# Kernel optimization log

Measured on AMD Instinct MI355X. Metric: run time of the kernel, lower is better.

Reference implementation:

```python
import jax, jax.numpy as jnp
import numpy as np
from jax import lax

KS = [3, 5, 7, 9]
DS = [1, 2, 3, 4]
BN_EPS = 1e-5


def setup_inputs() -> dict:
    key = jax.random.key(0)
    ks = jax.random.split(key, 16)
    B, Cin, H, W = 16, 64, 256, 256
    Ce = 64  # out_channels // 2
    inp = {"x": jax.random.normal(ks[0], (B, Cin, H, W), jnp.float32)}
    for i, (k, _) in enumerate(zip(KS, DS)):
        fan_in = Cin * k * k
        inp[f"w{i}"] = jax.random.normal(ks[1 + i], (Ce, Cin, k, k), jnp.float32) / np.sqrt(fan_in)
        inp[f"b{i}"] = jnp.zeros((Ce,), jnp.float32)
    inp["bn_scale"] = jnp.ones((4, Ce), jnp.float32)
    inp["bn_bias"] = jnp.zeros((4, Ce), jnp.float32)
    inp["bn_mean"] = jax.random.normal(ks[5], (4, Ce), jnp.float32) * 0.1
    inp["bn_var"] = jax.random.uniform(ks[6], (4, Ce), jnp.float32, 0.5, 1.5)
    inp["gate_w"] = jax.random.normal(ks[7], (4, Cin), jnp.float32) / np.sqrt(Cin)
    inp["gate_b"] = jnp.zeros((4,), jnp.float32)
    return inp


def _expert(x, w, b, scale, bias, mean, var, k, d):
    pad = d * (k - 1) // 2
    y = lax.conv_general_dilated(
        x, w, window_strides=(2, 2), padding=[(pad, pad), (pad, pad)],
        rhs_dilation=(d, d), dimension_numbers=("NCHW", "OIHW", "NCHW"))
    y = y + b[None, :, None, None]
    inv = scale * lax.rsqrt(var + BN_EPS)
    y = y * inv[None, :, None, None] + (bias - mean * inv)[None, :, None, None]
    return jax.nn.gelu(y, approximate=False)


def reference(x, w0, b0, w1, b1, w2, b2, w3, b3,
              bn_scale, bn_bias, bn_mean, bn_var, gate_w, gate_b):
    B = x.shape[0]
    # Gate: global average pool -> linear -> softmax -> top-2 renormalized
    pooled = x.mean(axis=(2, 3))                    # (B, Cin)
    gates = jax.nn.softmax(pooled @ gate_w.T + gate_b, axis=1)  # (B, 4)
    top2_w, top2_idx = lax.top_k(gates, 2)
    top2_w = top2_w / (top2_w.sum(axis=1, keepdims=True) + 1e-8)
    # Dense compute of all 4 experts (faithful to original module)
    ws, bs = [w0, w1, w2, w3], [b0, b1, b2, b3]
    outs = [
        _expert(x, ws[i], bs[i], bn_scale[i], bn_bias[i], bn_mean[i], bn_var[i], KS[i], DS[i])
        for i in range(4)
    ]
    E = jnp.stack(outs, axis=1)                     # (B, 4, Ce, H/2, W/2)
    sel = jnp.take_along_axis(E, top2_idx[:, :, None, None, None], axis=1)  # (B,2,Ce,h,w)
    weighted = sel * top2_w[:, :, None, None, None]
    # concat top-2 along channel dim == reshape (B,2,Ce,h,w) -> (B,2*Ce,h,w)
    Bc, two, Ce, h, w = weighted.shape
    return weighted.reshape(Bc, two * Ce, h, w)
```

## Files before the change

### kernel.cpp

```cpp
#include <hip/hip_runtime.h>
#include <hip/hip_bf16.h>
#include <math.h>

#define CIN 64
#define CE  64
#define HH  256
#define WW  256
#define OHW 128
#define PW  288
#define PH  288
#define WOFF 19600
#define TOFF (WOFF + 6144)

typedef __attribute__((ext_vector_type(8))) short bf16x8;
typedef __attribute__((ext_vector_type(4))) float f32x4;

static __device__ __forceinline__ unsigned short f2bf(float f) {
    __hip_bfloat16 h = __float2bfloat16(f);
    return *reinterpret_cast<unsigned short*>(&h);
}

#define GLOAD16(gsrc, ldst)                                                        \
    __builtin_amdgcn_global_load_lds(                                              \
        (const __attribute__((address_space(1))) void*)(gsrc),                     \
        (__attribute__((address_space(3))) void*)(ldst), 16, 0, 0)

template <bool PRE>
__global__ __launch_bounds__(256)
void poolcvt_kernel(const float* __restrict__ x, unsigned short* __restrict__ xbf,
                    float* __restrict__ partial) {
    int blk = blockIdx.x;
    int rc = blockIdx.y;
    int tid = threadIdx.x, lane = tid & 63, wv = tid >> 6;
    int c0 = lane * 4;
    const float* xb = x + (size_t)blk * 8 * (HH * WW);
    unsigned short* pl = xbf + (size_t)blk * (PW * PH) * 8;
    float s[8];
#pragma unroll
    for (int j = 0; j < 8; ++j) s[j] = 0.f;
#pragma unroll 1
    for (int rr = wv; rr < 32; rr += 4) {
        int h = rc * 32 + rr;
        float4 v[8];
#pragma unroll
        for (int j = 0; j < 8; ++j)
            v[j] = *reinterpret_cast<const float4*>(xb + (size_t)j * (HH * WW) + h * WW + c0);
#pragma unroll
        for (int j = 0; j < 8; ++j) s[j] += (v[j].x + v[j].y) + (v[j].z + v[j].w);
        if (PRE) {
            size_t o16 = ((size_t)(16 + h) * PW + 16 + c0);
            unsigned short u[4][8];
#pragma unroll
            for (int j = 0; j < 8; ++j) {
                u[0][j] = f2bf(v[j].x);
                u[1][j] = f2bf(v[j].y);
                u[2][j] = f2bf(v[j].z);
                u[3][j] = f2bf(v[j].w);
            }
#pragma unroll
            for (int cc = 0; cc < 4; ++cc)
                *reinterpret_cast<bf16x8*>(pl + (o16 + cc) * 8) =
                    *reinterpret_cast<const bf16x8*>(u[cc]);
        }
    }
    if (PRE) {
        bf16x8 z = (bf16x8)(short)0;
#pragma unroll 1
        for (int i = tid; i < 32 * 32; i += 256) {
            int rr = i >> 5, cc = i & 31;
            int pr = 16 + rc * 32 + rr;
            int pc = (cc < 16) ? cc : (256 + cc);
            *reinterpret_cast<bf16x8*>(pl + ((size_t)pr * PW + pc) * 8) = z;
        }
        if (rc == 0) {
#pragma unroll 1
            for (int i = tid; i < 16 * PW; i += 256)
                *reinterpret_cast<bf16x8*>(pl + (size_t)i * 8) = z;
        }
        if (rc == 7) {
#pragma unroll 1
            for (int i = tid; i < 16 * PW; i += 256)
                *reinterpret_cast<bf16x8*>(pl + ((size_t)(272 * PW) + i) * 8) = z;
        }
    }
#pragma unroll
    for (int j = 0; j < 8; ++j) {
#pragma unroll
        for (int m = 32; m >= 1; m >>= 1) s[j] += __shfl_xor(s[j], m, 64);
    }
    __shared__ float red[4][8];
    if (lane == 0) {
#pragma unroll
        for (int j = 0; j < 8; ++j) red[wv][j] = s[j];
    }
    __syncthreads();
    if (tid < 8) {
        int j = tid;
        float t = (red[0][j] + red[1][j]) + (red[2][j] + red[3][j]);
        partial[(blk * 8 + rc) * 8 + j] = t;
    }
}

__global__ __launch_bounds__(64)
void gate_kernel(const float* __restrict__ partial, const float* __restrict__ gw,
                 const float* __restrict__ gb, int* __restrict__ sel_idx,
                 float* __restrict__ sel_w) {
    int b = blockIdx.x;
    int c = threadIdx.x;
    float p = 0.f;
#pragma unroll
    for (int rc = 0; rc < 8; ++rc)
        p += partial[(((b * 8 + (c >> 3)) * 8) + rc) * 8 + (c & 7)];
    p *= (1.0f / (HH * WW));
    float l[4];
#pragma unroll
    for (int e = 0; e < 4; ++e) l[e] = p * gw[e * CIN + c];
#pragma unroll
    for (int m = 32; m >= 1; m >>= 1) {
#pragma unroll
        for (int e = 0; e < 4; ++e) l[e] += __shfl_xor(l[e], m, 64);
    }
    if (c == 0) {
        float g[4], s = 0.f;
#pragma unroll
        for (int e = 0; e < 4; ++e) l[e] += gb[e];
        float mx = fmaxf(fmaxf(l[0], l[1]), fmaxf(l[2], l[3]));
#pragma unroll
        for (int e = 0; e < 4; ++e) { g[e] = expf(l[e] - mx); s += g[e]; }
#pragma unroll
        for (int e = 0; e < 4; ++e) g[e] /= s;
        int i1 = 0;
        for (int e = 1; e < 4; ++e) if (g[e] > g[i1]) i1 = e;
        int i2 = -1;
        for (int e = 0; e < 4; ++e) {
            if (e == i1) continue;
            if (i2 < 0 || g[e] > g[i2]) i2 = e;
        }
        float den = g[i1] + g[i2] + 1e-8f;
        sel_idx[b * 2 + 0] = i1;
        sel_idx[b * 2 + 1] = i2;
        sel_w[b * 2 + 0] = g[i1] / den;
        sel_w[b * 2 + 1] = g[i2] / den;
    }
}

__global__ void order_kernel(const int* __restrict__ sel_idx, int* __restrict__ ord) {
    if (threadIdx.x == 0) {
        int pos = 0;
        const int pri[4] = {3, 2, 1, 0};
        for (int pi = 0; pi < 4; ++pi)
            for (int bs = 0; bs < 32; ++bs)
                if (sel_idx[bs] == pri[pi]) ord[pos++] = bs;
    }
}

__global__ __launch_bounds__(256)
void wprep_all_kernel(const float* __restrict__ w0, const float* __restrict__ w1,
                      const float* __restrict__ w2, const float* __restrict__ w3,
                      unsigned short* __restrict__ wq) {
    int cb = blockIdx.x;
    int y = blockIdx.y;
    const float* w;
    int g0, k, GE;
    size_t base;
    if (y < 3)       { w = w0; g0 = y;      k = 3; GE = 3;  base = 0; }
    else if (y < 10) { w = w1; g0 = y - 3;  k = 5; GE = 7;  base = 49152; }
    else if (y < 23) { w = w2; g0 = y - 10; k = 7; GE = 13; base = 163840; }
    else             { w = w3; g0 = y - 23; k = 9; GE = 21; base = 376832; }
    int k2 = k * k;
    int t = threadIdx.x, tl = t >> 6, co = t & 63;
    int tap = g0 * 4 + tl;
    unsigned short vals[8];
#pragma unroll
    for (int j = 0; j < 8; ++j) {
        float v = 0.f;
        if (tap < k2) v = w[(size_t)(co * CIN + cb * 8 + j) * k2 + tap];
        vals[j] = f2bf(v);
    }
    *reinterpret_cast<bf16x8*>(&wq[base + (size_t)(cb * GE + g0) * 2048 + t * 8]) =
        *reinterpret_cast<const bf16x8*>(vals);
}

template <int K, int D, int GE, bool EVEN, bool PRE>
__device__ __forceinline__ void conv_body(const float* __restrict__ xb,
                                          const unsigned short* __restrict__ xpb,
                                          const unsigned short* __restrict__ wq,
                                          unsigned short* __restrict__ lds,
                                          f32x4 acc[4][4],
                                          int ih0, int iw0, int lane, int wv, int tid) {
    constexpr int K2 = K * K;
    constexpr int TS = 31 + (K - 1) * D;
    constexpr int S = (TS + 1) / 2;
    constexpr int HPW = S * 8;
    constexpr int PITCH = 2 * HPW;
    constexpr int NRC = (TS + 1) / 2;
    constexpr int NEL = EVEN ? NRC * NRC : TS * 2 * S;
    constexpr int ITER = (NEL + 255) / 256;
    constexpr int DH = EVEN ? D / 2 : 0;
    constexpr size_t PLANE = (size_t)PW * PH * 8;
    constexpr int RSTEP = EVEN ? NRC * 16 : PITCH * 4;
    int p = lane & 15, hi = lane >> 4;

    if constexpr (PRE) {
        int gofs[ITER];
#pragma unroll
        for (int i = 0; i < ITER; ++i) {
            int idx = tid + i * 256;
            if (idx > NEL - 1) idx = NEL - 1;
            int ih, iw;
            if constexpr (EVEN) {
                int r = idx / NRC, c = idx - r * NRC;
                ih = ih0 + 16 + 2 * r;
                iw = iw0 + 16 + 2 * c;
            } else {
                int r = idx / (2 * S), rem = idx - r * (2 * S);
                int half = rem >= S ? 1 : 0;
                int sl = rem - half * S;
                int c = 2 * sl + half;
                if (c > TS - 1) c = TS - 1;
                ih = ih0 + 16 + r;
                iw = iw0 + 16 + c;
            }
            gofs[i] = (ih * PW + iw) * 8;
        }
        if (tid < 4 * GE) {
            int tapc = tid < K2 ? tid : K2 - 1;
            int kh = tapc / K, kw = tapc % K;
            int off;
            if constexpr (EVEN)
                off = (DH * kh * NRC + DH * kw) * 16;
            else
                off = D * kh * PITCH * 2 + (kw & 1) * HPW * 2 +
                      (((D * kw) - (kw & 1)) >> 1) * 16;
            *reinterpret_cast<int*>(&lds[TOFF + tid * 2]) = off;
        }
        __syncthreads();
        const int* tab = reinterpret_cast<const int*>(&lds[TOFF]);
        const char* ldsc = reinterpret_cast<const char*>(lds);
        int baseB = EVEN ? ((wv * 4 * NRC + p) * 16) : (wv * 16 * PITCH + p * 16);

#pragma unroll 1
        for (int cb = 0; cb < 8; ++cb) {
            __builtin_amdgcn_s_barrier();
            const unsigned short* xp = xpb + (size_t)cb * PLANE;
#pragma unroll
            for (int i = 0; i < ITER; ++i) {
                if (tid + i * 256 < NEL)
                    GLOAD16(xp + gofs[i], &lds[(tid + i * 256) * 8]);
            }
            const unsigned short* wcb = wq + (size_t)cb * GE * 2048;
            GLOAD16(wcb + tid * 8, &lds[WOFF + tid * 8]);
            GLOAD16(wcb + 2048 + tid * 8, &lds[WOFF + 2048 + tid * 8]);
            int toffCur = tab[hi];
#pragma unroll
            for (int g = 0; g < GE; ++g) {
                if (g == GE - 1) asm volatile("s_waitcnt vmcnt(0)" ::: "memory");
                else             asm volatile("s_waitcnt vmcnt(1)" ::: "memory");
                __builtin_amdgcn_s_barrier();
                if (g + 2 < GE)
                    GLOAD16(wcb + (size_t)(g + 2) * 2048 + tid * 8,
                            &lds[WOFF + ((g + 2) % 3) * 2048 + tid * 8]);
                int toffNext = (g + 1 < GE) ? tab[(g + 1) * 4 + hi] : 0;
                const unsigned short* wl = &lds[WOFF + (g % 3) * 2048 + hi * 512 + p * 8];
                bf16x8 a0 = *reinterpret_cast<const bf16x8*>(wl);
                bf16x8 a1 = *reinterpret_cast<const bf16x8*>(wl + 128);
                bf16x8 a2 = *reinterpret_cast<const bf16x8*>(wl + 256);
                bf16x8 a3 = *reinterpret_cast<const bf16x8*>(wl + 384);
                const char* bp = ldsc + (baseB + toffCur);
#pragma unroll
                for (int j = 0; j < 4; ++j) {
                    const bf16x8 bf = *reinterpret_cast<const bf16x8*>(bp + j * RSTEP);
                    acc[j][0] = __builtin_amdgcn_mfma_f32_16x16x32_bf16(a0, bf, acc[j][0], 0, 0, 0);
                    acc[j][1] = __builtin_amdgcn_mfma_f32_16x16x32_bf16(a1, bf, acc[j][1], 0, 0, 0);
                    acc[j][2] = __builtin_amdgcn_mfma_f32_16x16x32_bf16(a2, bf, acc[j][2], 0, 0, 0);
                    acc[j][3] = __builtin_amdgcn_mfma_f32_16x16x32_bf16(a3, bf, acc[j][3], 0, 0, 0);
                }
                toffCur = toffNext;
            }
        }
    } else {
#pragma unroll 1
        for (int cb = 0; cb < 8; ++cb) {
            __syncthreads();
            const float* xc8 = xb + (size_t)cb * 8 * (HH * WW);
#pragma unroll 1
            for (int idx = tid; idx < NEL; idx += 256) {
                int ih, iw;
                if constexpr (EVEN) {
                    int r = idx / NRC, c = idx - r * NRC;
                    ih = ih0 + 2 * r; iw = iw0 + 2 * c;
                } else {
                    int r = idx / (2 * S), rem = idx - r * (2 * S);
                    int half = rem >= S ? 1 : 0;
                    int sl = rem - half * S;
                    int c = min(2 * sl + half, TS - 1);
                    ih = ih0 + r; iw = iw0 + c;
                }
                int ihc = min(max(ih, 0), HH - 1), iwc = min(max(iw, 0), WW - 1);
                bool ok = ((unsigned)ih < (unsigned)HH) && ((unsigned)iw < (unsigned)WW);
                unsigned short u[8];
                const float* src = xc8 + ihc * WW + iwc;
#pragma unroll
                for (int j = 0; j < 8; ++j) u[j] = f2bf(ok ? src[(size_t)j * (HH * WW)] : 0.f);
                *reinterpret_cast<bf16x8*>(&lds[idx * 8]) = *reinterpret_cast<const bf16x8*>(u);
            }
            __syncthreads();
            const unsigned short* wcb = wq + (size_t)cb * GE * 2048;
#pragma unroll 2
            for (int g = 0; g < GE; ++g) {
                int tap = g * 4 + hi;
                int tapc = tap < K2 ? tap : K2 - 1;
                int kh = tapc / K, kw = tapc % K;
                const unsigned short* wg = wcb + g * 2048 + hi * 512;
                bf16x8 a0 = *reinterpret_cast<const bf16x8*>(wg + p * 8);
                bf16x8 a1 = *reinterpret_cast<const bf16x8*>(wg + 128 + p * 8);
                bf16x8 a2 = *reinterpret_cast<const bf16x8*>(wg + 256 + p * 8);
                bf16x8 a3 = *reinterpret_cast<const bf16x8*>(wg + 384 + p * 8);
                if constexpr (EVEN) {
                    int ec = p + (D / 2) * kw;
                    int erb = wv * 4 + (D / 2) * kh;
#pragma unroll
                    for (int j = 0; j < 4; ++j) {
                        const bf16x8 bf = *reinterpret_cast<const bf16x8*>(
                            &lds[((erb + j) * NRC + ec) * 8]);
                        acc[j][0] = __builtin_amdgcn_mfma_f32_16x16x32_bf16(a0, bf, acc[j][0], 0, 0, 0);
                        acc[j][1] = __builtin_amdgcn_mfma_f32_16x16x32_bf16(a1, bf, acc[j][1], 0, 0, 0);
                        acc[j][2] = __builtin_amdgcn_mfma_f32_16x16x32_bf16(a2, bf, acc[j][2], 0, 0, 0);
                        acc[j][3] = __builtin_amdgcn_mfma_f32_16x16x32_bf16(a3, bf, acc[j][3], 0, 0, 0);
                    }
                } else {
                    int ic = 2 * p + D * kw;
                    int bbase = (ic & 1) * HPW + (ic >> 1) * 8;
                    int irb = D * kh + wv * 8;
#pragma unroll
                    for (int j = 0; j < 4; ++j) {
                        const bf16x8 bf = *reinterpret_cast<const bf16x8*>(
                            &lds[(irb + 2 * j) * PITCH + bbase]);
                        acc[j][0] = __builtin_amdgcn_mfma_f32_16x16x32_bf16(a0, bf, acc[j][0], 0, 0, 0);
                        acc[j][1] = __builtin_amdgcn_mfma_f32_16x16x32_bf16(a1, bf, acc[j][1], 0, 0, 0);
                        acc[j][2] = __builtin_amdgcn_mfma_f32_16x16x32_bf16(a2, bf, acc[j][2], 0, 0, 0);
                        acc[j][3] = __builtin_amdgcn_mfma_f32_16x16x32_bf16(a3, bf, acc[j][3], 0, 0, 0);
                    }
                }
            }
        }
    }
}

template <bool PRE>
__global__ __launch_bounds__(256, 3)
void conv_moe_kernel(const float* __restrict__ x, const unsigned short* __restrict__ xbf,
                     const unsigned short* __restrict__ wq,
                     const float* __restrict__ b0_, const float* __restrict__ b1_,
                     const float* __restrict__ b2_, const float* __restrict__ b3_,
                     const float* __restrict__ bns, const float* __restrict__ bnb,
                     const float* __restrict__ bnm, const float* __restrict__ bnv,
                     const int* __restrict__ sel_idx, const float* __restrict__ sel_w,
                     const int* __restrict__ ord, float* __restrict__ out) {
    __shared__ __align__(16) unsigned short lds[TOFF + 176];

    int bidx = blockIdx.x;
    int bs = ord[bidx >> 6];
    int tile = bidx & 63;
    int b = bs >> 1, slot = bs & 1;
    int e = sel_idx[bs];
    float gwt = sel_w[bs];
    int oh0 = (tile >> 3) * 16, ow0 = (tile & 7) * 16;
    const float* xb = x + (size_t)b * CIN * HH * WW;
    const unsigned short* xpb = xbf + (size_t)b * 8 * (PW * PH) * 8;
    int tid = threadIdx.x, lane = tid & 63, wv = tid >> 6;
    int p = lane & 15, hi = lane >> 4;

    f32x4 acc[4][4];
#pragma unroll
    for (int j = 0; j < 4; ++j)
#pragma unroll
        for (int ct = 0; ct < 4; ++ct) acc[j][ct] = (f32x4){0.f, 0.f, 0.f, 0.f};

    switch (e) {
        case 0:
            conv_body<3, 1, 3, false, PRE>(xb, xpb, wq, lds, acc, oh0 * 2 - 1, ow0 * 2 - 1, lane, wv, tid);
            break;
        case 1:
            conv_body<5, 2, 7, true, PRE>(xb, xpb, wq + 49152, lds, acc, oh0 * 2 - 4, ow0 * 2 - 4, lane, wv, tid);
            break;
        case 2:
            conv_body<7, 3, 13, false, PRE>(xb, xpb, wq + 163840, lds, acc, oh0 * 2 - 9, ow0 * 2 - 9, lane, wv, tid);
            break;
        default:
            conv_body<9, 4, 21, true, PRE>(xb, xpb, wq + 376832, lds, acc, oh0 * 2 - 16, ow0 * 2 - 16, lane, wv, tid);
            break;
    }

    const float* be = (e == 0) ? b0_ : (e == 1) ? b1_ : (e == 2) ? b2_ : b3_;
    float* ob = out + (size_t)(b * 128 + slot * 64) * (OHW * OHW);
#pragma unroll
    for (int ct = 0; ct < 4; ++ct) {
#pragma unroll
        for (int reg = 0; reg < 4; ++reg) {
            int co = ct * 16 + hi * 4 + reg;
            float bias = be[co];
            float sc = bns[e * CE + co], bi = bnb[e * CE + co];
            float mn = bnm[e * CE + co], vr = bnv[e * CE + co];
            float inv = sc * rsqrtf(vr + 1e-5f);
            float beta = bi - mn * inv + bias * inv;
#pragma unroll
            for (int j = 0; j < 4; ++j) {
                float y = acc[j][ct][reg] * inv + beta;
                float gl = 0.5f * y * (1.0f + erff(y * 0.70710678118654752f));
                int oh = oh0 + wv * 4 + j, ow = ow0 + p;
                ob[(size_t)co * (OHW * OHW) + oh * OHW + ow] = gl * gwt;
            }
        }
    }
}

extern "C" void kernel_launch(void* const* d_in, const int* in_sizes, int n_in,
                              void* d_out, int out_size, void* d_ws, size_t ws_size,
                              hipStream_t stream) {
    const float* x   = (const float*)d_in[0];
    const float* w0  = (const float*)d_in[1];
    const float* b0  = (const float*)d_in[2];
    const float* w1  = (const float*)d_in[3];
    const float* b1  = (const float*)d_in[4];
    const float* w2  = (const float*)d_in[5];
    const float* b2  = (const float*)d_in[6];
    const float* w3  = (const float*)d_in[7];
    const float* b3  = (const float*)d_in[8];
    const float* bns = (const float*)d_in[9];
    const float* bnb = (const float*)d_in[10];
    const float* bnm = (const float*)d_in[11];
    const float* bnv = (const float*)d_in[12];
    const float* gw  = (const float*)d_in[13];
    const float* gb  = (const float*)d_in[14];
    float* out = (float*)d_out;

    char* ws = (char*)d_ws;
    float* partial = (float*)ws;
    int* sel_idx   = (int*)(ws + 32768);
    float* sel_w   = (float*)(ws + 32896);
    int* ord       = (int*)(ws + 33024);
    unsigned short* wq = (unsigned short*)(ws + 33280);
    unsigned short* xbf = (unsigned short*)(ws + 2097152);
    const size_t NEED = 2097152ull + (size_t)128 * PW * PH * 16;
    bool pre = ws_size >= NEED;

    if (pre) poolcvt_kernel<true><<<dim3(128, 8), 256, 0, stream>>>(x, xbf, partial);
    else     poolcvt_kernel<false><<<dim3(128, 8), 256, 0, stream>>>(x, xbf, partial);
    gate_kernel<<<dim3(16), 64, 0, stream>>>(partial, gw, gb, sel_idx, sel_w);
    order_kernel<<<dim3(1), 64, 0, stream>>>(sel_idx, ord);
    wprep_all_kernel<<<dim3(8, 44), 256, 0, stream>>>(w0, w1, w2, w3, wq);

    if (pre)
        conv_moe_kernel<true><<<dim3(2048), 256, 0, stream>>>(
            x, xbf, wq, b0, b1, b2, b3, bns, bnb, bnm, bnv, sel_idx, sel_w, ord, out);
    else
        conv_moe_kernel<false><<<dim3(2048), 256, 0, stream>>>(
            x, xbf, wq, b0, b1, b2, b3, bns, bnb, bnm, bnv, sel_idx, sel_w, ord, out);
}
```

Before: 271.7 us.

## Software-pipeline LDS fragment loads in conv MFMA loop and merge gate/order kernels

Restructures the inner tap loop of the conv kernel so the A/B fragments for tap g+1 are read from LDS while the MFMAs for tap g run, and raises wave priority around the MFMA block. The weight-buffer wait is changed to a full vmcnt(0) plus barrier at each step. Separately, the gate and order kernels are merged into one single-block launch that loops over the batch, removing one launch. Costs are more registers for the double-buffered fragments and a serialized gate computation.

```diff
diff --git a/kernel.cpp b/kernel.cpp
--- a/kernel.cpp
+++ b/kernel.cpp
@@ -102,50 +102,49 @@
 }
 
 __global__ __launch_bounds__(64)
-void gate_kernel(const float* __restrict__ partial, const float* __restrict__ gw,
-                 const float* __restrict__ gb, int* __restrict__ sel_idx,
-                 float* __restrict__ sel_w) {
-    int b = blockIdx.x;
+void gate_order_kernel(const float* __restrict__ partial, const float* __restrict__ gw,
+                       const float* __restrict__ gb, int* __restrict__ sel_idx,
+                       float* __restrict__ sel_w, int* __restrict__ ord) {
     int c = threadIdx.x;
-    float p = 0.f;
-#pragma unroll
-    for (int rc = 0; rc < 8; ++rc)
-        p += partial[(((b * 8 + (c >> 3)) * 8) + rc) * 8 + (c & 7)];
-    p *= (1.0f / (HH * WW));
-    float l[4];
-#pragma unroll
-    for (int e = 0; e < 4; ++e) l[e] = p * gw[e * CIN + c];
-#pragma unroll
-    for (int m = 32; m >= 1; m >>= 1) {
-#pragma unroll
-        for (int e = 0; e < 4; ++e) l[e] += __shfl_xor(l[e], m, 64);
+#pragma unroll 1
+    for (int b = 0; b < 16; ++b) {
+        float pq = 0.f;
+#pragma unroll
+        for (int rc = 0; rc < 8; ++rc)
+            pq += partial[(((b * 8 + (c >> 3)) * 8) + rc) * 8 + (c & 7)];
+        pq *= (1.0f / (HH * WW));
+        float l[4];
+#pragma unroll
+        for (int e = 0; e < 4; ++e) l[e] = pq * gw[e * CIN + c];
+#pragma unroll
+        for (int m = 32; m >= 1; m >>= 1) {
+#pragma unroll
+            for (int e = 0; e < 4; ++e) l[e] += __shfl_xor(l[e], m, 64);
+        }
+        if (c == 0) {
+            float g[4], s = 0.f;
+#pragma unroll
+            for (int e = 0; e < 4; ++e) l[e] += gb[e];
+            float mx = fmaxf(fmaxf(l[0], l[1]), fmaxf(l[2], l[3]));
+#pragma unroll
+            for (int e = 0; e < 4; ++e) { g[e] = expf(l[e] - mx); s += g[e]; }
+#pragma unroll
+            for (int e = 0; e < 4; ++e) g[e] /= s;
+            int i1 = 0;
+            for (int e = 1; e < 4; ++e) if (g[e] > g[i1]) i1 = e;
+            int i2 = -1;
+            for (int e = 0; e < 4; ++e) {
+                if (e == i1) continue;
+                if (i2 < 0 || g[e] > g[i2]) i2 = e;
+            }
+            float den = g[i1] + g[i2] + 1e-8f;
+            sel_idx[b * 2 + 0] = i1;
+            sel_idx[b * 2 + 1] = i2;
+            sel_w[b * 2 + 0] = g[i1] / den;
+            sel_w[b * 2 + 1] = g[i2] / den;
+        }
     }
     if (c == 0) {
-        float g[4], s = 0.f;
-#pragma unroll
-        for (int e = 0; e < 4; ++e) l[e] += gb[e];
-        float mx = fmaxf(fmaxf(l[0], l[1]), fmaxf(l[2], l[3]));
-#pragma unroll
-        for (int e = 0; e < 4; ++e) { g[e] = expf(l[e] - mx); s += g[e]; }
-#pragma unroll
-        for (int e = 0; e < 4; ++e) g[e] /= s;
-        int i1 = 0;
-        for (int e = 1; e < 4; ++e) if (g[e] > g[i1]) i1 = e;
-        int i2 = -1;
-        for (int e = 0; e < 4; ++e) {
-            if (e == i1) continue;
-            if (i2 < 0 || g[e] > g[i2]) i2 = e;
-        }
-        float den = g[i1] + g[i2] + 1e-8f;
-        sel_idx[b * 2 + 0] = i1;
-        sel_idx[b * 2 + 1] = i2;
-        sel_w[b * 2 + 0] = g[i1] / den;
-        sel_w[b * 2 + 1] = g[i2] / den;
-    }
-}
-
-__global__ void order_kernel(const int* __restrict__ sel_idx, int* __restrict__ ord) {
-    if (threadIdx.x == 0) {
         int pos = 0;
         const int pri[4] = {3, 2, 1, 0};
         for (int pi = 0; pi < 4; ++pi)
@@ -251,30 +250,69 @@
             const unsigned short* wcb = wq + (size_t)cb * GE * 2048;
             GLOAD16(wcb + tid * 8, &lds[WOFF + tid * 8]);
             GLOAD16(wcb + 2048 + tid * 8, &lds[WOFF + 2048 + tid * 8]);
+            asm volatile("s_waitcnt vmcnt(0)" ::: "memory");
+            __builtin_amdgcn_s_barrier();
+            GLOAD16(wcb + 2 * 2048 + tid * 8, &lds[WOFF + 2 * 2048 + tid * 8]);
             int toffCur = tab[hi];
+            bf16x8 A0, A1, A2, A3, B0, B1, B2, B3;
+            {
+                const unsigned short* wl = &lds[WOFF + hi * 512 + p * 8];
+                A0 = *reinterpret_cast<const bf16x8*>(wl);
+                A1 = *reinterpret_cast<const bf16x8*>(wl + 128);
+                A2 = *reinterpret_cast<const bf16x8*>(wl + 256);
+                A3 = *reinterpret_cast<const bf16x8*>(wl + 384);
+                const char* bp = ldsc + (baseB + toffCur);
+                B0 = *reinterpret_cast<const bf16x8*>(bp);
+                B1 = *reinterpret_cast<const bf16x8*>(bp + RSTEP);
+                B2 = *reinterpret_cast<const bf16x8*>(bp + 2 * RSTEP);
+                B3 = *reinterpret_cast<const bf16x8*>(bp + 3 * RSTEP);
+            }
 #pragma unroll
             for (int g = 0; g < GE; ++g) {
-                if (g == GE - 1) asm volatile("s_waitcnt vmcnt(0)" ::: "memory");
-                else             asm volatile("s_waitcnt vmcnt(1)" ::: "memory");
-                __builtin_amdgcn_s_barrier();
-                if (g + 2 < GE)
-                    GLOAD16(wcb + (size_t)(g + 2) * 2048 + tid * 8,
-                            &lds[WOFF + ((g + 2) % 3) * 2048 + tid * 8]);
-                int toffNext = (g + 1 < GE) ? tab[(g + 1) * 4 + hi] : 0;
-                const unsigned short* wl = &lds[WOFF + (g % 3) * 2048 + hi * 512 + p * 8];
-                bf16x8 a0 = *reinterpret_cast<const bf16x8*>(wl);
-                bf16x8 a1 = *reinterpret_cast<const bf16x8*>(wl + 128);
-                bf16x8 a2 = *reinterpret_cast<const bf16x8*>(wl + 256);
-                bf16x8 a3 = *reinterpret_cast<const bf16x8*>(wl + 384);
-                const char* bp = ldsc + (baseB + toffCur);
-#pragma unroll
-                for (int j = 0; j < 4; ++j) {
-                    const bf16x8 bf = *reinterpret_cast<const bf16x8*>(bp + j * RSTEP);
-                    acc[j][0] = __builtin_amdgcn_mfma_f32_16x16x32_bf16(a0, bf, acc[j][0], 0, 0, 0);
-                    acc[j][1] = __builtin_amdgcn_mfma_f32_16x16x32_bf16(a1, bf, acc[j][1], 0, 0, 0);
-                    acc[j][2] = __builtin_amdgcn_mfma_f32_16x16x32_bf16(a2, bf, acc[j][2], 0, 0, 0);
-                    acc[j][3] = __builtin_amdgcn_mfma_f32_16x16x32_bf16(a3, bf, acc[j][3], 0, 0, 0);
+                if (g >= 1) {
+                    asm volatile("s_waitcnt vmcnt(0)" ::: "memory");
+                    __builtin_amdgcn_s_barrier();
+                    if (g + 2 < GE)
+                        GLOAD16(wcb + (size_t)(g + 2) * 2048 + tid * 8,
+                                &lds[WOFF + ((g + 2) % 3) * 2048 + tid * 8]);
                 }
+                bf16x8 An0 = A0, An1 = A1, An2 = A2, An3 = A3;
+                bf16x8 Bn0 = B0, Bn1 = B1, Bn2 = B2, Bn3 = B3;
+                int toffNext = toffCur;
+                if (g + 1 < GE) {
+                    toffNext = tab[(g + 1) * 4 + hi];
+                    const unsigned short* wl =
+                        &lds[WOFF + ((g + 1) % 3) * 2048 + hi * 512 + p * 8];
+                    An0 = *reinterpret_cast<const bf16x8*>(wl);
+                    An1 = *reinterpret_cast<const bf16x8*>(wl + 128);
+                    An2 = *reinterpret_cast<const bf16x8*>(wl + 256);
+                    An3 = *reinterpret_cast<const bf16x8*>(wl + 384);
+                    const char* bpn = ldsc + (baseB + toffNext);
+                    Bn0 = *reinterpret_cast<const bf16x8*>(bpn);
+                    Bn1 = *reinterpret_cast<const bf16x8*>(bpn + RSTEP);
+                    Bn2 = *reinterpret_cast<const bf16x8*>(bpn + 2 * RSTEP);
+                    Bn3 = *reinterpret_cast<const bf16x8*>(bpn + 3 * RSTEP);
+                }
+                __builtin_amdgcn_s_setprio(1);
+                acc[0][0] = __builtin_amdgcn_mfma_f32_16x16x32_bf16(A0, B0, acc[0][0], 0, 0, 0);
+                acc[0][1] = __builtin_amdgcn_mfma_f32_16x16x32_bf16(A1, B0, acc[0][1], 0, 0, 0);
+                acc[0][2] = __builtin_amdgcn_mfma_f32_16x16x32_bf16(A2, B0, acc[0][2], 0, 0, 0);
+                acc[0][3] = __builtin_amdgcn_mfma_f32_16x16x32_bf16(A3, B0, acc[0][3], 0, 0, 0);
+                acc[1][0] = __builtin_amdgcn_mfma_f32_16x16x32_bf16(A0, B1, acc[1][0], 0, 0, 0);
+                acc[1][1] = __builtin_amdgcn_mfma_f32_16x16x32_bf16(A1, B1, acc[1][1], 0, 0, 0);
+                acc[1][2] = __builtin_amdgcn_mfma_f32_16x16x32_bf16(A2, B1, acc[1][2], 0, 0, 0);
+                acc[1][3] = __builtin_amdgcn_mfma_f32_16x16x32_bf16(A3, B1, acc[1][3], 0, 0, 0);
+                acc[2][0] = __builtin_amdgcn_mfma_f32_16x16x32_bf16(A0, B2, acc[2][0], 0, 0, 0);
+                acc[2][1] = __builtin_amdgcn_mfma_f32_16x16x32_bf16(A1, B2, acc[2][1], 0, 0, 0);
+                acc[2][2] = __builtin_amdgcn_mfma_f32_16x16x32_bf16(A2, B2, acc[2][2], 0, 0, 0);
+                acc[2][3] = __builtin_amdgcn_mfma_f32_16x16x32_bf16(A3, B2, acc[2][3], 0, 0, 0);
+                acc[3][0] = __builtin_amdgcn_mfma_f32_16x16x32_bf16(A0, B3, acc[3][0], 0, 0, 0);
+                acc[3][1] = __builtin_amdgcn_mfma_f32_16x16x32_bf16(A1, B3, acc[3][1], 0, 0, 0);
+                acc[3][2] = __builtin_amdgcn_mfma_f32_16x16x32_bf16(A2, B3, acc[3][2], 0, 0, 0);
+                acc[3][3] = __builtin_amdgcn_mfma_f32_16x16x32_bf16(A3, B3, acc[3][3], 0, 0, 0);
+                __builtin_amdgcn_s_setprio(0);
+                A0 = An0; A1 = An1; A2 = An2; A3 = An3;
+                B0 = Bn0; B1 = Bn1; B2 = Bn2; B3 = Bn3;
                 toffCur = toffNext;
             }
         }
@@ -447,8 +485,7 @@
 
     if (pre) poolcvt_kernel<true><<<dim3(128, 8), 256, 0, stream>>>(x, xbf, partial);
     else     poolcvt_kernel<false><<<dim3(128, 8), 256, 0, stream>>>(x, xbf, partial);
-    gate_kernel<<<dim3(16), 64, 0, stream>>>(partial, gw, gb, sel_idx, sel_w);
-    order_kernel<<<dim3(1), 64, 0, stream>>>(sel_idx, ord);
+    gate_order_kernel<<<dim3(1), 64, 0, stream>>>(partial, gw, gb, sel_idx, sel_w, ord);
     wprep_all_kernel<<<dim3(8, 44), 256, 0, stream>>>(w0, w1, w2, w3, wq);
 
     if (pre)
```

Result: slower. 292.0 us (+7.5%).

## Widen conv output tile to 16x32 and merge gate and order kernels

Applied to the files above, without the earlier changes.

Each conv block now computes a 16x32 output tile instead of 16x16. Every wave holds 8 accumulator rows, so each loaded weight fragment feeds twice as many MFMAs and the halo overhead per output drops. LDS grows past the static limit, so the kernel switches to dynamic shared memory with a raised attribute and occupancy drops from 3 to 2 blocks per CU. The gate and order kernels are fused into one single-block launch to save a launch.

```diff
diff --git a/kernel.cpp b/kernel.cpp
--- a/kernel.cpp
+++ b/kernel.cpp
@@ -9,8 +9,9 @@
 #define OHW 128
 #define PW  288
 #define PH  288
-#define WOFF 19600
+#define WOFF 32144
 #define TOFF (WOFF + 6144)
+#define SHMEM 76912
 
 typedef __attribute__((ext_vector_type(8))) short bf16x8;
 typedef __attribute__((ext_vector_type(4))) float f32x4;
@@ -102,50 +103,49 @@
 }
 
 __global__ __launch_bounds__(64)
-void gate_kernel(const float* __restrict__ partial, const float* __restrict__ gw,
-                 const float* __restrict__ gb, int* __restrict__ sel_idx,
-                 float* __restrict__ sel_w) {
-    int b = blockIdx.x;
+void gate_order_kernel(const float* __restrict__ partial, const float* __restrict__ gw,
+                       const float* __restrict__ gb, int* __restrict__ sel_idx,
+                       float* __restrict__ sel_w, int* __restrict__ ord) {
     int c = threadIdx.x;
-    float p = 0.f;
-#pragma unroll
-    for (int rc = 0; rc < 8; ++rc)
-        p += partial[(((b * 8 + (c >> 3)) * 8) + rc) * 8 + (c & 7)];
-    p *= (1.0f / (HH * WW));
-    float l[4];
-#pragma unroll
-    for (int e = 0; e < 4; ++e) l[e] = p * gw[e * CIN + c];
-#pragma unroll
-    for (int m = 32; m >= 1; m >>= 1) {
-#pragma unroll
-        for (int e = 0; e < 4; ++e) l[e] += __shfl_xor(l[e], m, 64);
+#pragma unroll 1
+    for (int b = 0; b < 16; ++b) {
+        float pq = 0.f;
+#pragma unroll
+        for (int rc = 0; rc < 8; ++rc)
+            pq += partial[(((b * 8 + (c >> 3)) * 8) + rc) * 8 + (c & 7)];
+        pq *= (1.0f / (HH * WW));
+        float l[4];
+#pragma unroll
+        for (int e = 0; e < 4; ++e) l[e] = pq * gw[e * CIN + c];
+#pragma unroll
+        for (int m = 32; m >= 1; m >>= 1) {
+#pragma unroll
+            for (int e = 0; e < 4; ++e) l[e] += __shfl_xor(l[e], m, 64);
+        }
+        if (c == 0) {
+            float g[4], s = 0.f;
+#pragma unroll
+            for (int e = 0; e < 4; ++e) l[e] += gb[e];
+            float mx = fmaxf(fmaxf(l[0], l[1]), fmaxf(l[2], l[3]));
+#pragma unroll
+            for (int e = 0; e < 4; ++e) { g[e] = expf(l[e] - mx); s += g[e]; }
+#pragma unroll
+            for (int e = 0; e < 4; ++e) g[e] /= s;
+            int i1 = 0;
+            for (int e = 1; e < 4; ++e) if (g[e] > g[i1]) i1 = e;
+            int i2 = -1;
+            for (int e = 0; e < 4; ++e) {
+                if (e == i1) continue;
+                if (i2 < 0 || g[e] > g[i2]) i2 = e;
+            }
+            float den = g[i1] + g[i2] + 1e-8f;
+            sel_idx[b * 2 + 0] = i1;
+            sel_idx[b * 2 + 1] = i2;
+            sel_w[b * 2 + 0] = g[i1] / den;
+            sel_w[b * 2 + 1] = g[i2] / den;
+        }
     }
     if (c == 0) {
-        float g[4], s = 0.f;
-#pragma unroll
-        for (int e = 0; e < 4; ++e) l[e] += gb[e];
-        float mx = fmaxf(fmaxf(l[0], l[1]), fmaxf(l[2], l[3]));
-#pragma unroll
-        for (int e = 0; e < 4; ++e) { g[e] = expf(l[e] - mx); s += g[e]; }
-#pragma unroll
-        for (int e = 0; e < 4; ++e) g[e] /= s;
-        int i1 = 0;
-        for (int e = 1; e < 4; ++e) if (g[e] > g[i1]) i1 = e;
-        int i2 = -1;
-        for (int e = 0; e < 4; ++e) {
-            if (e == i1) continue;
-            if (i2 < 0 || g[e] > g[i2]) i2 = e;
-        }
-        float den = g[i1] + g[i2] + 1e-8f;
-        sel_idx[b * 2 + 0] = i1;
-        sel_idx[b * 2 + 1] = i2;
-        sel_w[b * 2 + 0] = g[i1] / den;
-        sel_w[b * 2 + 1] = g[i2] / den;
-    }
-}
-
-__global__ void order_kernel(const int* __restrict__ sel_idx, int* __restrict__ ord) {
-    if (threadIdx.x == 0) {
         int pos = 0;
         const int pri[4] = {3, 2, 1, 0};
         for (int pi = 0; pi < 4; ++pi)
@@ -186,19 +186,20 @@
                                           const unsigned short* __restrict__ xpb,
                                           const unsigned short* __restrict__ wq,
                                           unsigned short* __restrict__ lds,
-                                          f32x4 acc[4][4],
+                                          f32x4 acc[8][4],
                                           int ih0, int iw0, int lane, int wv, int tid) {
     constexpr int K2 = K * K;
-    constexpr int TS = 31 + (K - 1) * D;
-    constexpr int S = (TS + 1) / 2;
+    constexpr int TS_H = 31 + (K - 1) * D;
+    constexpr int TS_W = 63 + (K - 1) * D;
+    constexpr int S = (TS_W + 1) / 2;
     constexpr int HPW = S * 8;
     constexpr int PITCH = 2 * HPW;
-    constexpr int NRC = (TS + 1) / 2;
-    constexpr int NEL = EVEN ? NRC * NRC : TS * 2 * S;
+    constexpr int NRH = (TS_H + 1) / 2, NRW = (TS_W + 1) / 2;
+    constexpr int NEL = EVEN ? NRH * NRW : TS_H * 2 * S;
     constexpr int ITER = (NEL + 255) / 256;
     constexpr int DH = EVEN ? D / 2 : 0;
     constexpr size_t PLANE = (size_t)PW * PH * 8;
-    constexpr int RSTEP = EVEN ? NRC * 16 : PITCH * 4;
+    constexpr int RSTEP = EVEN ? NRW * 16 : PITCH * 4;
     int p = lane & 15, hi = lane >> 4;
 
     if constexpr (PRE) {
@@ -209,7 +210,7 @@
             if (idx > NEL - 1) idx = NEL - 1;
             int ih, iw;
             if constexpr (EVEN) {
-                int r = idx / NRC, c = idx - r * NRC;
+                int r = idx / NRW, c = idx - r * NRW;
                 ih = ih0 + 16 + 2 * r;
                 iw = iw0 + 16 + 2 * c;
             } else {
@@ -217,7 +218,7 @@
                 int half = rem >= S ? 1 : 0;
                 int sl = rem - half * S;
                 int c = 2 * sl + half;
-                if (c > TS - 1) c = TS - 1;
+                if (c > TS_W - 1) c = TS_W - 1;
                 ih = ih0 + 16 + r;
                 iw = iw0 + 16 + c;
             }
@@ -228,7 +229,7 @@
             int kh = tapc / K, kw = tapc % K;
             int off;
             if constexpr (EVEN)
-                off = (DH * kh * NRC + DH * kw) * 16;
+                off = (DH * kh * NRW + DH * kw) * 16;
             else
                 off = D * kh * PITCH * 2 + (kw & 1) * HPW * 2 +
                       (((D * kw) - (kw & 1)) >> 1) * 16;
@@ -237,7 +238,7 @@
         __syncthreads();
         const int* tab = reinterpret_cast<const int*>(&lds[TOFF]);
         const char* ldsc = reinterpret_cast<const char*>(lds);
-        int baseB = EVEN ? ((wv * 4 * NRC + p) * 16) : (wv * 16 * PITCH + p * 16);
+        int baseB = EVEN ? ((wv * 4 * NRW + p) * 16) : (wv * 16 * PITCH + p * 16);
 
 #pragma unroll 1
         for (int cb = 0; cb < 8; ++cb) {
@@ -268,8 +269,10 @@
                 bf16x8 a3 = *reinterpret_cast<const bf16x8*>(wl + 384);
                 const char* bp = ldsc + (baseB + toffCur);
 #pragma unroll
-                for (int j = 0; j < 4; ++j) {
-                    const bf16x8 bf = *reinterpret_cast<const bf16x8*>(bp + j * RSTEP);
+                for (int j = 0; j < 8; ++j) {
+                    int jj = j >> 1, jh = j & 1;
+                    const bf16x8 bf =
+                        *reinterpret_cast<const bf16x8*>(bp + jj * RSTEP + jh * 256);
                     acc[j][0] = __builtin_amdgcn_mfma_f32_16x16x32_bf16(a0, bf, acc[j][0], 0, 0, 0);
                     acc[j][1] = __builtin_amdgcn_mfma_f32_16x16x32_bf16(a1, bf, acc[j][1], 0, 0, 0);
                     acc[j][2] = __builtin_amdgcn_mfma_f32_16x16x32_bf16(a2, bf, acc[j][2], 0, 0, 0);
@@ -287,13 +290,13 @@
             for (int idx = tid; idx < NEL; idx += 256) {
                 int ih, iw;
                 if constexpr (EVEN) {
-                    int r = idx / NRC, c = idx - r * NRC;
+                    int r = idx / NRW, c = idx - r * NRW;
                     ih = ih0 + 2 * r; iw = iw0 + 2 * c;
                 } else {
                     int r = idx / (2 * S), rem = idx - r * (2 * S);
                     int half = rem >= S ? 1 : 0;
                     int sl = rem - half * S;
-                    int c = min(2 * sl + half, TS - 1);
+                    int c = min(2 * sl + half, TS_W - 1);
                     ih = ih0 + r; iw = iw0 + c;
                 }
                 int ihc = min(max(ih, 0), HH - 1), iwc = min(max(iw, 0), WW - 1);
@@ -316,31 +319,25 @@
                 bf16x8 a1 = *reinterpret_cast<const bf16x8*>(wg + 128 + p * 8);
                 bf16x8 a2 = *reinterpret_cast<const bf16x8*>(wg + 256 + p * 8);
                 bf16x8 a3 = *reinterpret_cast<const bf16x8*>(wg + 384 + p * 8);
-                if constexpr (EVEN) {
-                    int ec = p + (D / 2) * kw;
-                    int erb = wv * 4 + (D / 2) * kh;
-#pragma unroll
-                    for (int j = 0; j < 4; ++j) {
-                        const bf16x8 bf = *reinterpret_cast<const bf16x8*>(
-                            &lds[((erb + j) * NRC + ec) * 8]);
-                        acc[j][0] = __builtin_amdgcn_mfma_f32_16x16x32_bf16(a0, bf, acc[j][0], 0, 0, 0);
-                        acc[j][1] = __builtin_amdgcn_mfma_f32_16x16x32_bf16(a1, bf, acc[j][1], 0, 0, 0);
-                        acc[j][2] = __builtin_amdgcn_mfma_f32_16x16x32_bf16(a2, bf, acc[j][2], 0, 0, 0);
-                        acc[j][3] = __builtin_amdgcn_mfma_f32_16x16x32_bf16(a3, bf, acc[j][3], 0, 0, 0);
+#pragma unroll
+                for (int j = 0; j < 8; ++j) {
+                    int jj = j >> 1, jh = j & 1;
+                    const bf16x8* bfp;
+                    if constexpr (EVEN) {
+                        int ec = p + (D / 2) * kw + jh * 16;
+                        int erb = wv * 4 + (D / 2) * kh + jj;
+                        bfp = reinterpret_cast<const bf16x8*>(&lds[(erb * NRW + ec) * 8]);
+                    } else {
+                        int ic = 2 * p + D * kw + 32 * jh;
+                        int bbase = (ic & 1) * HPW + (ic >> 1) * 8;
+                        int irb = D * kh + wv * 8 + 2 * jj;
+                        bfp = reinterpret_cast<const bf16x8*>(&lds[irb * PITCH + bbase]);
                     }
-                } else {
-                    int ic = 2 * p + D * kw;
-                    int bbase = (ic & 1) * HPW + (ic >> 1) * 8;
-                    int irb = D * kh + wv * 8;
-#pragma unroll
-                    for (int j = 0; j < 4; ++j) {
-                        const bf16x8 bf = *reinterpret_cast<const bf16x8*>(
-                            &lds[(irb + 2 * j) * PITCH + bbase]);
-                        acc[j][0] = __builtin_amdgcn_mfma_f32_16x16x32_bf16(a0, bf, acc[j][0], 0, 0, 0);
-                        acc[j][1] = __builtin_amdgcn_mfma_f32_16x16x32_bf16(a1, bf, acc[j][1], 0, 0, 0);
-                        acc[j][2] = __builtin_amdgcn_mfma_f32_16x16x32_bf16(a2, bf, acc[j][2], 0, 0, 0);
-                        acc[j][3] = __builtin_amdgcn_mfma_f32_16x16x32_bf16(a3, bf, acc[j][3], 0, 0, 0);
-                    }
+                    const bf16x8 bf = *bfp;
+                    acc[j][0] = __builtin_amdgcn_mfma_f32_16x16x32_bf16(a0, bf, acc[j][0], 0, 0, 0);
+                    acc[j][1] = __builtin_amdgcn_mfma_f32_16x16x32_bf16(a1, bf, acc[j][1], 0, 0, 0);
+                    acc[j][2] = __builtin_amdgcn_mfma_f32_16x16x32_bf16(a2, bf, acc[j][2], 0, 0, 0);
+                    acc[j][3] = __builtin_amdgcn_mfma_f32_16x16x32_bf16(a3, bf, acc[j][3], 0, 0, 0);
                 }
             }
         }
@@ -348,7 +345,7 @@
 }
 
 template <bool PRE>
-__global__ __launch_bounds__(256, 3)
+__global__ __launch_bounds__(256, 2)
 void conv_moe_kernel(const float* __restrict__ x, const unsigned short* __restrict__ xbf,
                      const unsigned short* __restrict__ wq,
                      const float* __restrict__ b0_, const float* __restrict__ b1_,
@@ -357,23 +354,23 @@
                      const float* __restrict__ bnm, const float* __restrict__ bnv,
                      const int* __restrict__ sel_idx, const float* __restrict__ sel_w,
                      const int* __restrict__ ord, float* __restrict__ out) {
-    __shared__ __align__(16) unsigned short lds[TOFF + 176];
+    extern __shared__ __align__(16) unsigned short lds[];
 
     int bidx = blockIdx.x;
-    int bs = ord[bidx >> 6];
-    int tile = bidx & 63;
+    int bs = ord[bidx >> 5];
+    int tile = bidx & 31;
     int b = bs >> 1, slot = bs & 1;
     int e = sel_idx[bs];
     float gwt = sel_w[bs];
-    int oh0 = (tile >> 3) * 16, ow0 = (tile & 7) * 16;
+    int oh0 = (tile >> 2) * 16, ow0 = (tile & 3) * 32;
     const float* xb = x + (size_t)b * CIN * HH * WW;
     const unsigned short* xpb = xbf + (size_t)b * 8 * (PW * PH) * 8;
     int tid = threadIdx.x, lane = tid & 63, wv = tid >> 6;
     int p = lane & 15, hi = lane >> 4;
 
-    f32x4 acc[4][4];
-#pragma unroll
-    for (int j = 0; j < 4; ++j)
+    f32x4 acc[8][4];
+#pragma unroll
+    for (int j = 0; j < 8; ++j)
 #pragma unroll
         for (int ct = 0; ct < 4; ++ct) acc[j][ct] = (f32x4){0.f, 0.f, 0.f, 0.f};
 
@@ -405,10 +402,11 @@
             float inv = sc * rsqrtf(vr + 1e-5f);
             float beta = bi - mn * inv + bias * inv;
 #pragma unroll
-            for (int j = 0; j < 4; ++j) {
+            for (int j = 0; j < 8; ++j) {
+                int jj = j >> 1, jh = j & 1;
                 float y = acc[j][ct][reg] * inv + beta;
                 float gl = 0.5f * y * (1.0f + erff(y * 0.70710678118654752f));
-                int oh = oh0 + wv * 4 + j, ow = ow0 + p;
+                int oh = oh0 + wv * 4 + jj, ow = ow0 + jh * 16 + p;
                 ob[(size_t)co * (OHW * OHW) + oh * OHW + ow] = gl * gwt;
             }
         }
@@ -445,16 +443,20 @@
     const size_t NEED = 2097152ull + (size_t)128 * PW * PH * 16;
     bool pre = ws_size >= NEED;
 
+    hipFuncSetAttribute(reinterpret_cast<const void*>(&conv_moe_kernel<true>),
+                        hipFuncAttributeMaxDynamicSharedMemorySize, SHMEM);
+    hipFuncSetAttribute(reinterpret_cast<const void*>(&conv_moe_kernel<false>),
+                        hipFuncAttributeMaxDynamicSharedMemorySize, SHMEM);
+
     if (pre) poolcvt_kernel<true><<<dim3(128, 8), 256, 0, stream>>>(x, xbf, partial);
     else     poolcvt_kernel<false><<<dim3(128, 8), 256, 0, stream>>>(x, xbf, partial);
-    gate_kernel<<<dim3(16), 64, 0, stream>>>(partial, gw, gb, sel_idx, sel_w);
-    order_kernel<<<dim3(1), 64, 0, stream>>>(sel_idx, ord);
+    gate_order_kernel<<<dim3(1), 64, 0, stream>>>(partial, gw, gb, sel_idx, sel_w, ord);
     wprep_all_kernel<<<dim3(8, 44), 256, 0, stream>>>(w0, w1, w2, w3, wq);
 
     if (pre)
-        conv_moe_kernel<true><<<dim3(2048), 256, 0, stream>>>(
+        conv_moe_kernel<true><<<dim3(1024), 256, SHMEM, stream>>>(
             x, xbf, wq, b0, b1, b2, b3, bns, bnb, bnm, bnv, sel_idx, sel_w, ord, out);
     else
-        conv_moe_kernel<false><<<dim3(2048), 256, 0, stream>>>(
+        conv_moe_kernel<false><<<dim3(1024), 256, SHMEM, stream>>>(
             x, xbf, wq, b0, b1, b2, b3, bns, bnb, bnm, bnv, sel_idx, sel_w, ord, out);
 }
```

Result: slower. 284.2 us (+4.6%).

## Software-pipeline LDS operand reads with double-buffered registers in MFMA conv loop

Applied to the files above, without the earlier changes.

Restructures the inner tap loop so the A and B operand reads from LDS for the next tap are issued in inline assembly before the MFMAs of the current tap, using two register sets that alternate. The tap offset table is prefetched two steps ahead, waits and barriers move to the end of each step, and s_setprio raises priority around the MFMA block. The goal is to hide LDS latency behind matrix math. In exchange it uses more vector registers, which may lower occupancy, and it relies on hand-placed waitcnt that is easy to get wrong.

```diff
diff --git a/kernel.cpp b/kernel.cpp
--- a/kernel.cpp
+++ b/kernel.cpp
@@ -15,9 +15,15 @@
 typedef __attribute__((ext_vector_type(8))) short bf16x8;
 typedef __attribute__((ext_vector_type(4))) float f32x4;
 
+struct OpsT { bf16x8 a0, a1, a2, a3, b0, b1, b2, b3; };
+
 static __device__ __forceinline__ unsigned short f2bf(float f) {
     __hip_bfloat16 h = __float2bfloat16(f);
     return *reinterpret_cast<unsigned short*>(&h);
+}
+
+static __device__ __forceinline__ unsigned ldsaddr(const unsigned short* p) {
+    return (unsigned)(size_t)(const __attribute__((address_space(3))) unsigned short*)p;
 }
 
 #define GLOAD16(gsrc, ldst)                                                        \
@@ -235,13 +241,24 @@
             *reinterpret_cast<int*>(&lds[TOFF + tid * 2]) = off;
         }
         __syncthreads();
-        const int* tab = reinterpret_cast<const int*>(&lds[TOFF]);
-        const char* ldsc = reinterpret_cast<const char*>(lds);
-        int baseB = EVEN ? ((wv * 4 * NRC + p) * 16) : (wv * 16 * PITCH + p * 16);
+
+        unsigned aA0 = ldsaddr(&lds[WOFF + 0 * 2048 + hi * 512 + p * 8]);
+        unsigned aA1 = ldsaddr(&lds[WOFF + 1 * 2048 + hi * 512 + p * 8]);
+        unsigned aA2 = ldsaddr(&lds[WOFF + 2 * 2048 + hi * 512 + p * 8]);
+        unsigned baseB = EVEN ? (unsigned)((wv * 4 * NRC + p) * 16)
+                              : (unsigned)(wv * 16 * PITCH + p * 16);
+        unsigned xt0 = ldsaddr(&lds[0]);
+        unsigned bb0 = xt0 + baseB + 0 * RSTEP;
+        unsigned bb1 = xt0 + baseB + 1 * RSTEP;
+        unsigned bb2 = xt0 + baseB + 2 * RSTEP;
+        unsigned bb3 = xt0 + baseB + 3 * RSTEP;
+        unsigned tabhi = ldsaddr(&lds[TOFF]) + (unsigned)(hi * 4);
+
+        OpsT E, O;
+        int t0 = 0, t1 = 0;
 
 #pragma unroll 1
         for (int cb = 0; cb < 8; ++cb) {
-            __builtin_amdgcn_s_barrier();
             const unsigned short* xp = xpb + (size_t)cb * PLANE;
 #pragma unroll
             for (int i = 0; i < ITER; ++i) {
@@ -251,31 +268,86 @@
             const unsigned short* wcb = wq + (size_t)cb * GE * 2048;
             GLOAD16(wcb + tid * 8, &lds[WOFF + tid * 8]);
             GLOAD16(wcb + 2048 + tid * 8, &lds[WOFF + 2048 + tid * 8]);
-            int toffCur = tab[hi];
+            int toff0;
+            asm volatile("ds_read_b32 %0, %2\n\t"
+                         "ds_read_b32 %1, %2 offset:16"
+                         : "=&v"(toff0), "=&v"(t1)
+                         : "v"(tabhi));
+            asm volatile("s_waitcnt vmcnt(0) lgkmcnt(0)" ::: "memory");
+            __builtin_amdgcn_s_barrier();
+            {
+                unsigned c0 = bb0 + (unsigned)toff0, c1 = bb1 + (unsigned)toff0;
+                unsigned c2 = bb2 + (unsigned)toff0, c3 = bb3 + (unsigned)toff0;
+                asm volatile("ds_read_b128 %0, %4\n\t"
+                             "ds_read_b128 %1, %4 offset:256\n\t"
+                             "ds_read_b128 %2, %4 offset:512\n\t"
+                             "ds_read_b128 %3, %4 offset:768"
+                             : "=&v"(E.a0), "=&v"(E.a1), "=&v"(E.a2), "=&v"(E.a3)
+                             : "v"(aA0));
+                asm volatile("ds_read_b128 %0, %4\n\t"
+                             "ds_read_b128 %1, %5\n\t"
+                             "ds_read_b128 %2, %6\n\t"
+                             "ds_read_b128 %3, %7"
+                             : "=&v"(E.b0), "=&v"(E.b1), "=&v"(E.b2), "=&v"(E.b3)
+                             : "v"(c0), "v"(c1), "v"(c2), "v"(c3));
+            }
+            asm volatile("s_waitcnt lgkmcnt(0)" ::: "memory");
+            __builtin_amdgcn_sched_barrier(0);
+
 #pragma unroll
             for (int g = 0; g < GE; ++g) {
-                if (g == GE - 1) asm volatile("s_waitcnt vmcnt(0)" ::: "memory");
-                else             asm volatile("s_waitcnt vmcnt(1)" ::: "memory");
-                __builtin_amdgcn_s_barrier();
+                OpsT& cur = (g & 1) ? O : E;
+                OpsT& nxt = (g & 1) ? E : O;
                 if (g + 2 < GE)
                     GLOAD16(wcb + (size_t)(g + 2) * 2048 + tid * 8,
                             &lds[WOFF + ((g + 2) % 3) * 2048 + tid * 8]);
-                int toffNext = (g + 1 < GE) ? tab[(g + 1) * 4 + hi] : 0;
-                const unsigned short* wl = &lds[WOFF + (g % 3) * 2048 + hi * 512 + p * 8];
-                bf16x8 a0 = *reinterpret_cast<const bf16x8*>(wl);
-                bf16x8 a1 = *reinterpret_cast<const bf16x8*>(wl + 128);
-                bf16x8 a2 = *reinterpret_cast<const bf16x8*>(wl + 256);
-                bf16x8 a3 = *reinterpret_cast<const bf16x8*>(wl + 384);
-                const char* bp = ldsc + (baseB + toffCur);
-#pragma unroll
-                for (int j = 0; j < 4; ++j) {
-                    const bf16x8 bf = *reinterpret_cast<const bf16x8*>(bp + j * RSTEP);
-                    acc[j][0] = __builtin_amdgcn_mfma_f32_16x16x32_bf16(a0, bf, acc[j][0], 0, 0, 0);
-                    acc[j][1] = __builtin_amdgcn_mfma_f32_16x16x32_bf16(a1, bf, acc[j][1], 0, 0, 0);
-                    acc[j][2] = __builtin_amdgcn_mfma_f32_16x16x32_bf16(a2, bf, acc[j][2], 0, 0, 0);
-                    acc[j][3] = __builtin_amdgcn_mfma_f32_16x16x32_bf16(a3, bf, acc[j][3], 0, 0, 0);
+                if (g + 1 < GE) {
+                    int tN = (g & 1) ? t0 : t1;
+                    unsigned aAn = ((g + 1) % 3 == 0) ? aA0 : ((g + 1) % 3 == 1) ? aA1 : aA2;
+                    unsigned c0 = bb0 + (unsigned)tN, c1 = bb1 + (unsigned)tN;
+                    unsigned c2 = bb2 + (unsigned)tN, c3 = bb3 + (unsigned)tN;
+                    asm volatile("ds_read_b128 %0, %4\n\t"
+                                 "ds_read_b128 %1, %4 offset:256\n\t"
+                                 "ds_read_b128 %2, %4 offset:512\n\t"
+                                 "ds_read_b128 %3, %4 offset:768"
+                                 : "=&v"(nxt.a0), "=&v"(nxt.a1), "=&v"(nxt.a2), "=&v"(nxt.a3)
+                                 : "v"(aAn));
+                    asm volatile("ds_read_b128 %0, %4\n\t"
+                                 "ds_read_b128 %1, %5\n\t"
+                                 "ds_read_b128 %2, %6\n\t"
+                                 "ds_read_b128 %3, %7"
+                                 : "=&v"(nxt.b0), "=&v"(nxt.b1), "=&v"(nxt.b2), "=&v"(nxt.b3)
+                                 : "v"(c0), "v"(c1), "v"(c2), "v"(c3));
                 }
-                toffCur = toffNext;
+                if (g + 2 < GE) {
+                    unsigned tAg = tabhi + (unsigned)((g + 2) * 16);
+                    if (g & 1)
+                        asm volatile("ds_read_b32 %0, %1" : "=&v"(t1) : "v"(tAg));
+                    else
+                        asm volatile("ds_read_b32 %0, %1" : "=&v"(t0) : "v"(tAg));
+                }
+                __builtin_amdgcn_s_setprio(1);
+                acc[0][0] = __builtin_amdgcn_mfma_f32_16x16x32_bf16(cur.a0, cur.b0, acc[0][0], 0, 0, 0);
+                acc[0][1] = __builtin_amdgcn_mfma_f32_16x16x32_bf16(cur.a1, cur.b0, acc[0][1], 0, 0, 0);
+                acc[0][2] = __builtin_amdgcn_mfma_f32_16x16x32_bf16(cur.a2, cur.b0, acc[0][2], 0, 0, 0);
+                acc[0][3] = __builtin_amdgcn_mfma_f32_16x16x32_bf16(cur.a3, cur.b0, acc[0][3], 0, 0, 0);
+                acc[1][0] = __builtin_amdgcn_mfma_f32_16x16x32_bf16(cur.a0, cur.b1, acc[1][0], 0, 0, 0);
+                acc[1][1] = __builtin_amdgcn_mfma_f32_16x16x32_bf16(cur.a1, cur.b1, acc[1][1], 0, 0, 0);
+                acc[1][2] = __builtin_amdgcn_mfma_f32_16x16x32_bf16(cur.a2, cur.b1, acc[1][2], 0, 0, 0);
+                acc[1][3] = __builtin_amdgcn_mfma_f32_16x16x32_bf16(cur.a3, cur.b1, acc[1][3], 0, 0, 0);
+                acc[2][0] = __builtin_amdgcn_mfma_f32_16x16x32_bf16(cur.a0, cur.b2, acc[2][0], 0, 0, 0);
+                acc[2][1] = __builtin_amdgcn_mfma_f32_16x16x32_bf16(cur.a1, cur.b2, acc[2][1], 0, 0, 0);
+                acc[2][2] = __builtin_amdgcn_mfma_f32_16x16x32_bf16(cur.a2, cur.b2, acc[2][2], 0, 0, 0);
+                acc[2][3] = __builtin_amdgcn_mfma_f32_16x16x32_bf16(cur.a3, cur.b2, acc[2][3], 0, 0, 0);
+                acc[3][0] = __builtin_amdgcn_mfma_f32_16x16x32_bf16(cur.a0, cur.b3, acc[3][0], 0, 0, 0);
+                acc[3][1] = __builtin_amdgcn_mfma_f32_16x16x32_bf16(cur.a1, cur.b3, acc[3][1], 0, 0, 0);
+                acc[3][2] = __builtin_amdgcn_mfma_f32_16x16x32_bf16(cur.a2, cur.b3, acc[3][2], 0, 0, 0);
+                acc[3][3] = __builtin_amdgcn_mfma_f32_16x16x32_bf16(cur.a3, cur.b3, acc[3][3], 0, 0, 0);
+                __builtin_amdgcn_s_setprio(0);
+                asm volatile("s_waitcnt vmcnt(0)" ::: "memory");
+                __builtin_amdgcn_s_barrier();
+                asm volatile("s_waitcnt lgkmcnt(0)" ::: "memory");
+                __builtin_amdgcn_sched_barrier(0);
             }
         }
     } else {
```

Measured after the change: 293.9 us. +8.2%, slower.
